# Kernel tuning notes

Measured on AMD Instinct MI355X. Metric: run time of the kernel, lower is better.

## Reference

```python
import jax, jax.numpy as jnp
import numpy as np

N = 100000      # nodes
E = 1600000     # edges (avg degree 16)
DIN = 128       # input_dim
DH = 128        # hidden_dim


def setup_inputs() -> dict:
    key = jax.random.key(0)
    ks = jax.random.split(key, 8)
    x = jax.random.normal(ks[0], (N, DIN), dtype=jnp.float32)
    edge_index = jax.random.randint(ks[1], (2, E), 0, N, dtype=jnp.int32)
    s_in = 1.0 / np.sqrt(DIN)
    s_h = 1.0 / np.sqrt(DH)
    # PyG SAGEConv: out = lin_l(mean_aggr(x_src)) + lin_r(x_dst); lin_l has bias, lin_r does not.
    w1l = jax.random.normal(ks[2], (DIN, DH), dtype=jnp.float32) * s_in
    b1l = jnp.zeros((DH,), dtype=jnp.float32)
    w1r = jax.random.normal(ks[3], (DIN, DH), dtype=jnp.float32) * s_in
    w2l = jax.random.normal(ks[4], (DH, DH), dtype=jnp.float32) * s_h
    b2l = jnp.zeros((DH,), dtype=jnp.float32)
    w2r = jax.random.normal(ks[5], (DH, DH), dtype=jnp.float32) * s_h
    return {"x": x, "edge_index": edge_index, "w1l": w1l, "b1l": b1l,
            "w1r": w1r, "w2l": w2l, "b2l": b2l, "w2r": w2r}


def sage_conv(x, edge_index, wl, bl, wr):
    # edge_index[0] = source, edge_index[1] = target (PyG source_to_target flow)
    row, col = edge_index[0], edge_index[1]
    num_nodes = x.shape[0]
    agg = jax.ops.segment_sum(x[row], col, num_segments=num_nodes)          # [N, d]
    deg = jax.ops.segment_sum(jnp.ones((row.shape[0],), x.dtype), col,
                              num_segments=num_nodes)                        # [N]
    mean = agg / jnp.maximum(deg, 1.0)[:, None]
    return mean @ wl + bl + x @ wr


def reference(x, edge_index, w1l, b1l, w1r, w2l, b2l, w2r):
    h = jax.nn.relu(sage_conv(x, edge_index, w1l, b1l, w1r))
    return jax.nn.relu(sage_conv(h, edge_index, w2l, b2l, w2r))
```

## Files before the change

kernel.cpp:

```cpp
#include <hip/hip_runtime.h>

#define D 128
#define BM 128
#define NWG 256

typedef short short8 __attribute__((ext_vector_type(8)));
typedef float f32x4 __attribute__((ext_vector_type(4)));

__device__ inline unsigned short f2bf_rne(float x) {
    unsigned int b = __float_as_uint(x);
    unsigned int r = (b + 0x7FFFu + ((b >> 16) & 1u)) >> 16;
    return (unsigned short)r;
}
__device__ inline float bf2f(unsigned short h) {
    return __uint_as_float(((unsigned int)h) << 16);
}
__device__ inline void acc_bf(float4& a, ushort4 u) {
    a.x += __uint_as_float((unsigned int)u.x << 16);
    a.y += __uint_as_float((unsigned int)u.y << 16);
    a.z += __uint_as_float((unsigned int)u.z << 16);
    a.w += __uint_as_float((unsigned int)u.w << 16);
}

__global__ __launch_bounds__(256) void convert_x(const float* __restrict__ x,
                                                 unsigned short* __restrict__ xb,
                                                 int total) {
    int i = (blockIdx.x * 256 + threadIdx.x) * 8;
    if (i < total) {
        float4 a = *reinterpret_cast<const float4*>(x + i);
        float4 b = *reinterpret_cast<const float4*>(x + i + 4);
        ushort4 u0, u1;
        u0.x = f2bf_rne(a.x); u0.y = f2bf_rne(a.y); u0.z = f2bf_rne(a.z); u0.w = f2bf_rne(a.w);
        u1.x = f2bf_rne(b.x); u1.y = f2bf_rne(b.y); u1.z = f2bf_rne(b.z); u1.w = f2bf_rne(b.w);
        *reinterpret_cast<ushort4*>(xb + i) = u0;
        *reinterpret_cast<ushort4*>(xb + i + 4) = u1;
    }
}


__global__ void scan1(const int* __restrict__ in, int* __restrict__ out,
                      int* __restrict__ bsum, int n) {
    __shared__ int s[256];
    int t = threadIdx.x;
    int i = blockIdx.x * 256 + t;
    int v = (i < n) ? in[i] : 0;
    s[t] = v;
    __syncthreads();
    #pragma unroll
    for (int off = 1; off < 256; off <<= 1) {
        int add = (t >= off) ? s[t - off] : 0;
        __syncthreads();
        s[t] += add;
        __syncthreads();
    }
    if (i < n) out[i] = s[t] - v;
    if (t == 255) bsum[blockIdx.x] = s[255];
}

__global__ void scan2(int* __restrict__ bsum, int nb) {
    __shared__ int s[512];
    int t = threadIdx.x;
    int v = (t < nb) ? bsum[t] : 0;
    s[t] = v;
    __syncthreads();
    #pragma unroll
    for (int off = 1; off < 512; off <<= 1) {
        int add = (t >= off) ? s[t - off] : 0;
        __syncthreads();
        s[t] += add;
        __syncthreads();
    }
    if (t < nb) bsum[t] = s[t] - v;
}

__global__ void scan3b(int* __restrict__ out, const int* __restrict__ bsum, int n) {
    int i = blockIdx.x * blockDim.x + threadIdx.x;
    if (i < n) out[i] += bsum[i >> 8];
}

__global__ void set_end(int* __restrict__ row_ptr, int n, int e) {
    row_ptr[n] = e;
}


__global__ __launch_bounds__(256) void hist_bucket(const int* __restrict__ coli,
                                                   int* __restrict__ hist_t,
                                                   int e, int nbkt, int cpw) {
    __shared__ int hist[512];
    int w = blockIdx.x, tid = threadIdx.x;
    for (int b = tid; b < nbkt; b += 256) hist[b] = 0;
    __syncthreads();
    int i1 = min((w + 1) * cpw, e);
    for (int i = w * cpw + tid; i < i1; i += 256)
        atomicAdd(&hist[coli[i] >> 8], 1);
    __syncthreads();
    for (int b = tid; b < nbkt; b += 256) hist_t[b * NWG + w] = hist[b];
}

__global__ __launch_bounds__(256) void scatter_bucket(const int* __restrict__ rowi,
                                                      const int* __restrict__ coli,
                                                      const int* __restrict__ scanned,
                                                      unsigned int* __restrict__ ebuf,
                                                      int e, int nbkt, int cpw) {
    __shared__ int cur[512];
    int w = blockIdx.x, tid = threadIdx.x;
    for (int b = tid; b < nbkt; b += 256) cur[b] = scanned[b * NWG + w];
    __syncthreads();
    int i1 = min((w + 1) * cpw, e);
    for (int i = w * cpw + tid; i < i1; i += 256) {
        int c = coli[i];
        int b = c >> 8;
        int p = atomicAdd(&cur[b], 1);
        ebuf[p] = ((unsigned int)rowi[i] << 8) | (unsigned int)(c & 255);
    }
}

__global__ __launch_bounds__(256) void csr_bucket(const int* __restrict__ scanned,
                                                  const unsigned int* __restrict__ ebuf,
                                                  int* __restrict__ row_ptr,
                                                  int* __restrict__ srcs,
                                                  int e, int n, int nbkt) {
    __shared__ int cnt[256], s[256], cur[256];
    int b = blockIdx.x, tid = threadIdx.x;
    int S = scanned[b * NWG];
    int Send = (b == nbkt - 1) ? e : scanned[(b + 1) * NWG];
    cnt[tid] = 0;
    __syncthreads();
    for (int i = S + tid; i < Send; i += 256)
        atomicAdd(&cnt[ebuf[i] & 255], 1);
    __syncthreads();
    int v = cnt[tid];
    s[tid] = v;
    __syncthreads();
    #pragma unroll
    for (int off = 1; off < 256; off <<= 1) {
        int add = (tid >= off) ? s[tid - off] : 0;
        __syncthreads();
        s[tid] += add;
        __syncthreads();
    }
    int offx = s[tid] - v;
    int node = b * 256 + tid;
    if (node < n) row_ptr[node] = S + offx;
    cur[tid] = offx;
    __syncthreads();
    for (int i = S + tid; i < Send; i += 256) {
        unsigned int pe = ebuf[i];
        int lc = (int)(pe & 255u);
        int p = S + atomicAdd(&cur[lc], 1);
        srcs[p] = (int)(pe >> 8);
    }
}

__global__ __launch_bounds__(256) void aggregate_mean_bf16(
    const unsigned short* __restrict__ xb, float* __restrict__ mean,
    const int* __restrict__ row_ptr, const int* __restrict__ srcs, int n) {
    int node = blockIdx.x * 4 + (threadIdx.x >> 6);
    if (node >= n) return;
    int lane = threadIdx.x & 63;
    int half = lane >> 5;
    int l32 = lane & 31;
    int beg = row_ptr[node];
    int end = row_ptr[node + 1];

    float4 ac[8];
    #pragma unroll
    for (int k = 0; k < 8; ++k) ac[k] = make_float4(0.f, 0.f, 0.f, 0.f);

    int j = beg;
    for (; j + 16 <= end; j += 16) {
        int sr[8];
        #pragma unroll
        for (int k = 0; k < 8; ++k) sr[k] = srcs[j + 2 * k + half];
        ushort4 v[8];
        #pragma unroll
        for (int k = 0; k < 8; ++k)
            v[k] = *reinterpret_cast<const ushort4*>(xb + (size_t)sr[k] * D + l32 * 4);
        #pragma unroll
        for (int k = 0; k < 8; ++k) acc_bf(ac[k], v[k]);
    }
    if (j + 8 <= end) {
        int sr[4];
        #pragma unroll
        for (int k = 0; k < 4; ++k) sr[k] = srcs[j + 2 * k + half];
        ushort4 v[4];
        #pragma unroll
        for (int k = 0; k < 4; ++k)
            v[k] = *reinterpret_cast<const ushort4*>(xb + (size_t)sr[k] * D + l32 * 4);
        #pragma unroll
        for (int k = 0; k < 4; ++k) acc_bf(ac[k], v[k]);
        j += 8;
    }
    if (j + 4 <= end) {
        ushort4 v0 = *reinterpret_cast<const ushort4*>(xb + (size_t)srcs[j + half] * D + l32 * 4);
        ushort4 v1 = *reinterpret_cast<const ushort4*>(xb + (size_t)srcs[j + 2 + half] * D + l32 * 4);
        acc_bf(ac[0], v0);
        acc_bf(ac[1], v1);
        j += 4;
    }
    if (j + 2 <= end) {
        ushort4 v0 = *reinterpret_cast<const ushort4*>(xb + (size_t)srcs[j + half] * D + l32 * 4);
        acc_bf(ac[0], v0);
        j += 2;
    }
    if (j < end && half == 0) {
        ushort4 v0 = *reinterpret_cast<const ushort4*>(xb + (size_t)srcs[j] * D + l32 * 4);
        acc_bf(ac[0], v0);
    }
    #pragma unroll
    for (int k = 4; k >= 1; k >>= 1)
        #pragma unroll
        for (int m = 0; m < k; ++m) {
            ac[m].x += ac[m + k].x; ac[m].y += ac[m + k].y;
            ac[m].z += ac[m + k].z; ac[m].w += ac[m + k].w;
        }
    ac[0].x += __shfl_xor(ac[0].x, 32, 64);
    ac[0].y += __shfl_xor(ac[0].y, 32, 64);
    ac[0].z += __shfl_xor(ac[0].z, 32, 64);
    ac[0].w += __shfl_xor(ac[0].w, 32, 64);

    if (half == 0) {
        float inv = 1.0f / fmaxf((float)(end - beg), 1.0f);
        float4 o;
        o.x = ac[0].x * inv; o.y = ac[0].y * inv; o.z = ac[0].z * inv; o.w = ac[0].w * inv;
        *reinterpret_cast<float4*>(mean + (size_t)node * D + l32 * 4) = o;
    }
}

__global__ __launch_bounds__(256) void split_w(const float* __restrict__ w1l,
                                               const float* __restrict__ w1r,
                                               const float* __restrict__ w2l,
                                               const float* __restrict__ w2r,
                                               short* __restrict__ wt) {
    int b = blockIdx.x;
    int layer = b >> 7;
    int nn = b & 127;
    int k = threadIdx.x;
    const float* wl = layer ? w2l : w1l;
    const float* wr = layer ? w2r : w1r;
    float v = (k < 128) ? wl[k * D + nn] : wr[(k - 128) * D + nn];
    unsigned short h = f2bf_rne(v);
    float lo = v - bf2f(h);
    unsigned short l = f2bf_rne(lo);
    short* base = wt + layer * 65536;
    base[nn * 256 + k] = (short)h;
    base[32768 + nn * 256 + k] = (short)l;
}

__global__ __launch_bounds__(256, 2) void sage_mm_mfma(
    const float* __restrict__ mean, const float* __restrict__ xin,
    const short* __restrict__ wth, const short* __restrict__ wtl,
    const float* __restrict__ bias, float* __restrict__ out,
    unsigned short* __restrict__ hbout, int n) {
    __shared__ short sAh[128 * 40];
    __shared__ short sAl[128 * 40];
    __shared__ short sBh[128 * 40];
    __shared__ short sBl[128 * 40];
    const int tid = threadIdx.x;
    const int wave = tid >> 6;
    const int lane = tid & 63;
    const int l15 = lane & 15;
    const int kg = lane >> 4;
    const int row0 = blockIdx.x * BM;

    f32x4 acc[2][8];
    #pragma unroll
    for (int fr = 0; fr < 2; ++fr)
        #pragma unroll
        for (int fc = 0; fc < 8; ++fc)
            acc[fr][fc] = (f32x4){0.f, 0.f, 0.f, 0.f};

    float4 pa[4];
    int4 pbh[2], pbl[2];

    #pragma unroll
    for (int i = 0; i < 4; ++i) {
        int f = tid + i * 256;
        int row = f >> 3, k4 = f & 7;
        int gr = row0 + row;
        pa[i] = (gr < n) ? *reinterpret_cast<const float4*>(&mean[(size_t)gr * D + k4 * 4])
                         : make_float4(0.f, 0.f, 0.f, 0.f);
    }
    #pragma unroll
    for (int i = 0; i < 2; ++i) {
        int f = tid + i * 256;
        int n_ = f >> 2, kq = f & 3;
        pbh[i] = *reinterpret_cast<const int4*>(&wth[n_ * 256 + kq * 8]);
        pbl[i] = *reinterpret_cast<const int4*>(&wtl[n_ * 256 + kq * 8]);
    }

    for (int c = 0; c < 8; ++c) {
        #pragma unroll
        for (int i = 0; i < 4; ++i) {
            int f = tid + i * 256;
            int row = f >> 3, k4 = f & 7;
            const float* pv = &pa[i].x;
            unsigned short h[4], l[4];
            #pragma unroll
            for (int j = 0; j < 4; ++j) {
                float v = pv[j];
                h[j] = f2bf_rne(v);
                l[j] = f2bf_rne(v - bf2f(h[j]));
            }
            short* dsth = &sAh[row * 40 + k4 * 4];
            short* dstl = &sAl[row * 40 + k4 * 4];
            #pragma unroll
            for (int j = 0; j < 4; ++j) { dsth[j] = (short)h[j]; dstl[j] = (short)l[j]; }
        }
        #pragma unroll
        for (int i = 0; i < 2; ++i) {
            int f = tid + i * 256;
            int n_ = f >> 2, kq = f & 3;
            *reinterpret_cast<int4*>(&sBh[n_ * 40 + kq * 8]) = pbh[i];
            *reinterpret_cast<int4*>(&sBl[n_ * 40 + kq * 8]) = pbl[i];
        }
        __syncthreads();

        if (c < 7) {
            const float* __restrict__ anext = (c + 1 < 4) ? mean : xin;
            const int ka = ((c + 1) & 3) * 32;
            const int kb = (c + 1) * 32;
            #pragma unroll
            for (int i = 0; i < 4; ++i) {
                int f = tid + i * 256;
                int row = f >> 3, k4 = f & 7;
                int gr = row0 + row;
                pa[i] = (gr < n) ? *reinterpret_cast<const float4*>(&anext[(size_t)gr * D + ka + k4 * 4])
                                 : make_float4(0.f, 0.f, 0.f, 0.f);
            }
            #pragma unroll
            for (int i = 0; i < 2; ++i) {
                int f = tid + i * 256;
                int n_ = f >> 2, kq = f & 3;
                pbh[i] = *reinterpret_cast<const int4*>(&wth[n_ * 256 + kb + kq * 8]);
                pbl[i] = *reinterpret_cast<const int4*>(&wtl[n_ * 256 + kb + kq * 8]);
            }
        }

        short8 ah[2], al[2];
        #pragma unroll
        for (int fr = 0; fr < 2; ++fr) {
            int r = wave * 32 + fr * 16 + l15;
            ah[fr] = *reinterpret_cast<const short8*>(&sAh[r * 40 + kg * 8]);
            al[fr] = *reinterpret_cast<const short8*>(&sAl[r * 40 + kg * 8]);
        }
        #pragma unroll
        for (int fc = 0; fc < 8; ++fc) {
            int cc = fc * 16 + l15;
            short8 bh = *reinterpret_cast<const short8*>(&sBh[cc * 40 + kg * 8]);
            short8 bl = *reinterpret_cast<const short8*>(&sBl[cc * 40 + kg * 8]);
            #pragma unroll
            for (int fr = 0; fr < 2; ++fr) {
                acc[fr][fc] = __builtin_amdgcn_mfma_f32_16x16x32_bf16(ah[fr], bh, acc[fr][fc], 0, 0, 0);
                acc[fr][fc] = __builtin_amdgcn_mfma_f32_16x16x32_bf16(al[fr], bh, acc[fr][fc], 0, 0, 0);
                acc[fr][fc] = __builtin_amdgcn_mfma_f32_16x16x32_bf16(ah[fr], bl, acc[fr][fc], 0, 0, 0);
            }
        }
        __syncthreads();
    }

    float bz[8];
    #pragma unroll
    for (int fc = 0; fc < 8; ++fc) bz[fc] = bias[fc * 16 + l15];
    #pragma unroll
    for (int fr = 0; fr < 2; ++fr) {
        #pragma unroll
        for (int j = 0; j < 4; ++j) {
            int gr = row0 + wave * 32 + fr * 16 + kg * 4 + j;
            if (gr < n) {
                #pragma unroll
                for (int fc = 0; fc < 8; ++fc) {
                    float v = fmaxf(acc[fr][fc][j] + bz[fc], 0.f);
                    out[(size_t)gr * D + fc * 16 + l15] = v;
                    if (hbout) hbout[(size_t)gr * D + fc * 16 + l15] = f2bf_rne(v);
                }
            }
        }
    }
}


extern "C" void kernel_launch(void* const* d_in, const int* in_sizes, int n_in,
                              void* d_out, int out_size, void* d_ws, size_t ws_size,
                              hipStream_t stream) {
    const float* x   = (const float*)d_in[0];
    const int*   ei  = (const int*)d_in[1];
    const float* w1l = (const float*)d_in[2];
    const float* b1l = (const float*)d_in[3];
    const float* w1r = (const float*)d_in[4];
    const float* w2l = (const float*)d_in[5];
    const float* b2l = (const float*)d_in[6];
    const float* w2r = (const float*)d_in[7];
    float* out = (float*)d_out;

    const int n = in_sizes[0] / D;
    const int e = in_sizes[1] / 2;
    const int* rowi = ei;
    const int* coli = ei + e;

    const int nbkt = (n + 255) >> 8;
    const int n2 = nbkt * NWG;
    const int cpw = (e + NWG - 1) / NWG;
    const int nb2 = n2 / 256;
    const int PN = ((n + 1 + 63) / 64) * 64;
    const int total = n * D;

    int* row_ptr  = (int*)d_ws;
    int* hist_t   = row_ptr + PN;
    int* scanned  = hist_t + n2;
    int* bsum     = scanned + n2;
    int* srcs     = bsum + 512;
    short* wt     = (short*)(srcs + e);
    float* mean   = (float*)(wt + 4 * 32768);
    unsigned short* xhb = (unsigned short*)(mean + (size_t)total);
    unsigned int* ebuf  = (unsigned int*)mean;

    convert_x<<<(total / 8 + 255) / 256, 256, 0, stream>>>(x, xhb, total);
    split_w<<<256, 256, 0, stream>>>(w1l, w1r, w2l, w2r, wt);

    hist_bucket<<<NWG, 256, 0, stream>>>(coli, hist_t, e, nbkt, cpw);
    scan1<<<nb2, 256, 0, stream>>>(hist_t, scanned, bsum, n2);
    scan2<<<1, 512, 0, stream>>>(bsum, nb2);
    scan3b<<<nb2, 256, 0, stream>>>(scanned, bsum, n2);
    scatter_bucket<<<NWG, 256, 0, stream>>>(rowi, coli, scanned, ebuf, e, nbkt, cpw);
    csr_bucket<<<nbkt, 256, 0, stream>>>(scanned, ebuf, row_ptr, srcs, e, n, nbkt);
    set_end<<<1, 1, 0, stream>>>(row_ptr, n, e);

    const int mm_grid = (n + BM - 1) / BM;

    aggregate_mean_bf16<<<(n + 3) / 4, 256, 0, stream>>>(xhb, mean, row_ptr, srcs, n);
    sage_mm_mfma<<<mm_grid, 256, 0, stream>>>(mean, x, wt, wt + 32768, b1l, out, xhb, n);

    aggregate_mean_bf16<<<(n + 3) / 4, 256, 0, stream>>>(xhb, mean, row_ptr, srcs, n);
    sage_mm_mfma<<<mm_grid, 256, 0, stream>>>(mean, out, wt + 65536, wt + 98304, b2l, out, nullptr, n);
}
```

Baseline: 442.1 us.

## Fuse neighbor mean aggregation into the MFMA SAGE GEMM kernel

Merges the gather-mean kernel and the split-bf16 MFMA GEMM into one kernel per layer. Each block aggregates 64 node rows straight into LDS as hi/lo bf16, so the fp32 mean buffer is never written to or read back from global memory. Layer 1 now stores its output only as hi/lo bf16 pairs, which layer 2 consumes directly, and the block tile shrinks to 64 rows with transposed MFMA operands so the epilogue can use vectorized stores. The costs are less GEMM reuse per block and a gather phase and MFMA phase that are serialized inside each block, which may hurt latency hiding.

```diff
diff --git a/kernel.cpp b/kernel.cpp
--- a/kernel.cpp
+++ b/kernel.cpp
@@ -1,7 +1,9 @@
 #include <hip/hip_runtime.h>
 
 #define D 128
-#define BM 128
+#define BM 64
+#define LDM 136
+#define LDC 40
 #define NWG 256
 
 typedef short short8 __attribute__((ext_vector_type(8)));
@@ -149,81 +151,6 @@
         int lc = (int)(pe & 255u);
         int p = S + atomicAdd(&cur[lc], 1);
         srcs[p] = (int)(pe >> 8);
-    }
-}
-
-__global__ __launch_bounds__(256) void aggregate_mean_bf16(
-    const unsigned short* __restrict__ xb, float* __restrict__ mean,
-    const int* __restrict__ row_ptr, const int* __restrict__ srcs, int n) {
-    int node = blockIdx.x * 4 + (threadIdx.x >> 6);
-    if (node >= n) return;
-    int lane = threadIdx.x & 63;
-    int half = lane >> 5;
-    int l32 = lane & 31;
-    int beg = row_ptr[node];
-    int end = row_ptr[node + 1];
-
-    float4 ac[8];
-    #pragma unroll
-    for (int k = 0; k < 8; ++k) ac[k] = make_float4(0.f, 0.f, 0.f, 0.f);
-
-    int j = beg;
-    for (; j + 16 <= end; j += 16) {
-        int sr[8];
-        #pragma unroll
-        for (int k = 0; k < 8; ++k) sr[k] = srcs[j + 2 * k + half];
-        ushort4 v[8];
-        #pragma unroll
-        for (int k = 0; k < 8; ++k)
-            v[k] = *reinterpret_cast<const ushort4*>(xb + (size_t)sr[k] * D + l32 * 4);
-        #pragma unroll
-        for (int k = 0; k < 8; ++k) acc_bf(ac[k], v[k]);
-    }
-    if (j + 8 <= end) {
-        int sr[4];
-        #pragma unroll
-        for (int k = 0; k < 4; ++k) sr[k] = srcs[j + 2 * k + half];
-        ushort4 v[4];
-        #pragma unroll
-        for (int k = 0; k < 4; ++k)
-            v[k] = *reinterpret_cast<const ushort4*>(xb + (size_t)sr[k] * D + l32 * 4);
-        #pragma unroll
-        for (int k = 0; k < 4; ++k) acc_bf(ac[k], v[k]);
-        j += 8;
-    }
-    if (j + 4 <= end) {
-        ushort4 v0 = *reinterpret_cast<const ushort4*>(xb + (size_t)srcs[j + half] * D + l32 * 4);
-        ushort4 v1 = *reinterpret_cast<const ushort4*>(xb + (size_t)srcs[j + 2 + half] * D + l32 * 4);
-        acc_bf(ac[0], v0);
-        acc_bf(ac[1], v1);
-        j += 4;
-    }
-    if (j + 2 <= end) {
-        ushort4 v0 = *reinterpret_cast<const ushort4*>(xb + (size_t)srcs[j + half] * D + l32 * 4);
-        acc_bf(ac[0], v0);
-        j += 2;
-    }
-    if (j < end && half == 0) {
-        ushort4 v0 = *reinterpret_cast<const ushort4*>(xb + (size_t)srcs[j] * D + l32 * 4);
-        acc_bf(ac[0], v0);
-    }
-    #pragma unroll
-    for (int k = 4; k >= 1; k >>= 1)
-        #pragma unroll
-        for (int m = 0; m < k; ++m) {
-            ac[m].x += ac[m + k].x; ac[m].y += ac[m + k].y;
-            ac[m].z += ac[m + k].z; ac[m].w += ac[m + k].w;
-        }
-    ac[0].x += __shfl_xor(ac[0].x, 32, 64);
-    ac[0].y += __shfl_xor(ac[0].y, 32, 64);
-    ac[0].z += __shfl_xor(ac[0].z, 32, 64);
-    ac[0].w += __shfl_xor(ac[0].w, 32, 64);
-
-    if (half == 0) {
-        float inv = 1.0f / fmaxf((float)(end - beg), 1.0f);
-        float4 o;
-        o.x = ac[0].x * inv; o.y = ac[0].y * inv; o.z = ac[0].z * inv; o.w = ac[0].w * inv;
-        *reinterpret_cast<float4*>(mean + (size_t)node * D + l32 * 4) = o;
     }
 }
 
@@ -247,40 +174,30 @@
     base[32768 + nn * 256 + k] = (short)l;
 }
 
-__global__ __launch_bounds__(256, 2) void sage_mm_mfma(
-    const float* __restrict__ mean, const float* __restrict__ xin,
+__global__ __launch_bounds__(256, 2) void fused_sage(
+    const unsigned short* __restrict__ gsrc,
+    const float* __restrict__ xf,
+    const unsigned short* __restrict__ xh,
+    const unsigned short* __restrict__ xl,
     const short* __restrict__ wth, const short* __restrict__ wtl,
-    const float* __restrict__ bias, float* __restrict__ out,
-    unsigned short* __restrict__ hbout, int n) {
-    __shared__ short sAh[128 * 40];
-    __shared__ short sAl[128 * 40];
-    __shared__ short sBh[128 * 40];
-    __shared__ short sBl[128 * 40];
+    const float* __restrict__ bias,
+    const int* __restrict__ row_ptr, const int* __restrict__ srcs,
+    float* __restrict__ outf,
+    unsigned short* __restrict__ hh, unsigned short* __restrict__ hl,
+    int n) {
+    __shared__ unsigned short mh[BM * LDM], ml[BM * LDM];
+    __shared__ short sAh[BM * LDC], sAl[BM * LDC];
+    __shared__ short sBh[128 * LDC], sBl[128 * LDC];
     const int tid = threadIdx.x;
     const int wave = tid >> 6;
     const int lane = tid & 63;
     const int l15 = lane & 15;
     const int kg = lane >> 4;
+    const int half = lane >> 5;
+    const int l32 = lane & 31;
     const int row0 = blockIdx.x * BM;
 
-    f32x4 acc[2][8];
-    #pragma unroll
-    for (int fr = 0; fr < 2; ++fr)
-        #pragma unroll
-        for (int fc = 0; fc < 8; ++fc)
-            acc[fr][fc] = (f32x4){0.f, 0.f, 0.f, 0.f};
-
-    float4 pa[4];
     int4 pbh[2], pbl[2];
-
-    #pragma unroll
-    for (int i = 0; i < 4; ++i) {
-        int f = tid + i * 256;
-        int row = f >> 3, k4 = f & 7;
-        int gr = row0 + row;
-        pa[i] = (gr < n) ? *reinterpret_cast<const float4*>(&mean[(size_t)gr * D + k4 * 4])
-                         : make_float4(0.f, 0.f, 0.f, 0.f);
-    }
     #pragma unroll
     for (int i = 0; i < 2; ++i) {
         int f = tid + i * 256;
@@ -289,45 +206,126 @@
         pbl[i] = *reinterpret_cast<const int4*>(&wtl[n_ * 256 + kq * 8]);
     }
 
+    for (int rr = 0; rr < 16; ++rr) {
+        int r = wave * 16 + rr;
+        int gr = row0 + r;
+        if (gr < n) {
+            int beg = row_ptr[gr];
+            int end = row_ptr[gr + 1];
+            float4 ac[8];
+            #pragma unroll
+            for (int k = 0; k < 8; ++k) ac[k] = make_float4(0.f, 0.f, 0.f, 0.f);
+            int j = beg;
+            for (; j + 16 <= end; j += 16) {
+                int sr[8];
+                #pragma unroll
+                for (int k = 0; k < 8; ++k) sr[k] = srcs[j + 2 * k + half];
+                ushort4 v[8];
+                #pragma unroll
+                for (int k = 0; k < 8; ++k)
+                    v[k] = *reinterpret_cast<const ushort4*>(gsrc + (size_t)sr[k] * D + l32 * 4);
+                #pragma unroll
+                for (int k = 0; k < 8; ++k) acc_bf(ac[k], v[k]);
+            }
+            if (j + 8 <= end) {
+                int sr[4];
+                #pragma unroll
+                for (int k = 0; k < 4; ++k) sr[k] = srcs[j + 2 * k + half];
+                ushort4 v[4];
+                #pragma unroll
+                for (int k = 0; k < 4; ++k)
+                    v[k] = *reinterpret_cast<const ushort4*>(gsrc + (size_t)sr[k] * D + l32 * 4);
+                #pragma unroll
+                for (int k = 0; k < 4; ++k) acc_bf(ac[k], v[k]);
+                j += 8;
+            }
+            if (j + 4 <= end) {
+                ushort4 v0 = *reinterpret_cast<const ushort4*>(gsrc + (size_t)srcs[j + half] * D + l32 * 4);
+                ushort4 v1 = *reinterpret_cast<const ushort4*>(gsrc + (size_t)srcs[j + 2 + half] * D + l32 * 4);
+                acc_bf(ac[0], v0);
+                acc_bf(ac[1], v1);
+                j += 4;
+            }
+            if (j + 2 <= end) {
+                ushort4 v0 = *reinterpret_cast<const ushort4*>(gsrc + (size_t)srcs[j + half] * D + l32 * 4);
+                acc_bf(ac[0], v0);
+                j += 2;
+            }
+            if (j < end && half == 0) {
+                ushort4 v0 = *reinterpret_cast<const ushort4*>(gsrc + (size_t)srcs[j] * D + l32 * 4);
+                acc_bf(ac[0], v0);
+            }
+            #pragma unroll
+            for (int k = 4; k >= 1; k >>= 1)
+                #pragma unroll
+                for (int m = 0; m < k; ++m) {
+                    ac[m].x += ac[m + k].x; ac[m].y += ac[m + k].y;
+                    ac[m].z += ac[m + k].z; ac[m].w += ac[m + k].w;
+                }
+            ac[0].x += __shfl_xor(ac[0].x, 32, 64);
+            ac[0].y += __shfl_xor(ac[0].y, 32, 64);
+            ac[0].z += __shfl_xor(ac[0].z, 32, 64);
+            ac[0].w += __shfl_xor(ac[0].w, 32, 64);
+            if (half == 0) {
+                float inv = 1.0f / fmaxf((float)(end - beg), 1.0f);
+                float m0 = ac[0].x * inv, m1 = ac[0].y * inv;
+                float m2 = ac[0].z * inv, m3 = ac[0].w * inv;
+                ushort4 uh, ul;
+                uh.x = f2bf_rne(m0); ul.x = f2bf_rne(m0 - bf2f(uh.x));
+                uh.y = f2bf_rne(m1); ul.y = f2bf_rne(m1 - bf2f(uh.y));
+                uh.z = f2bf_rne(m2); ul.z = f2bf_rne(m2 - bf2f(uh.z));
+                uh.w = f2bf_rne(m3); ul.w = f2bf_rne(m3 - bf2f(uh.w));
+                *reinterpret_cast<ushort4*>(&mh[r * LDM + l32 * 4]) = uh;
+                *reinterpret_cast<ushort4*>(&ml[r * LDM + l32 * 4]) = ul;
+            }
+        } else if (half == 0) {
+            ushort4 z = {0, 0, 0, 0};
+            *reinterpret_cast<ushort4*>(&mh[r * LDM + l32 * 4]) = z;
+            *reinterpret_cast<ushort4*>(&ml[r * LDM + l32 * 4]) = z;
+        }
+    }
+    __syncthreads();
+
+    f32x4 acc[8];
+    #pragma unroll
+    for (int fc = 0; fc < 8; ++fc) acc[fc] = (f32x4){0.f, 0.f, 0.f, 0.f};
+
+    float4 pda[2];
+    int4 pdh, pdl;
+
     for (int c = 0; c < 8; ++c) {
-        #pragma unroll
-        for (int i = 0; i < 4; ++i) {
-            int f = tid + i * 256;
-            int row = f >> 3, k4 = f & 7;
-            const float* pv = &pa[i].x;
-            unsigned short h[4], l[4];
-            #pragma unroll
-            for (int j = 0; j < 4; ++j) {
-                float v = pv[j];
-                h[j] = f2bf_rne(v);
-                l[j] = f2bf_rne(v - bf2f(h[j]));
-            }
-            short* dsth = &sAh[row * 40 + k4 * 4];
-            short* dstl = &sAl[row * 40 + k4 * 4];
-            #pragma unroll
-            for (int j = 0; j < 4; ++j) { dsth[j] = (short)h[j]; dstl[j] = (short)l[j]; }
-        }
         #pragma unroll
         for (int i = 0; i < 2; ++i) {
             int f = tid + i * 256;
             int n_ = f >> 2, kq = f & 3;
-            *reinterpret_cast<int4*>(&sBh[n_ * 40 + kq * 8]) = pbh[i];
-            *reinterpret_cast<int4*>(&sBl[n_ * 40 + kq * 8]) = pbl[i];
+            *reinterpret_cast<int4*>(&sBh[n_ * LDC + kq * 8]) = pbh[i];
+            *reinterpret_cast<int4*>(&sBl[n_ * LDC + kq * 8]) = pbl[i];
+        }
+        if (c >= 4) {
+            if (xf) {
+                #pragma unroll
+                for (int i = 0; i < 2; ++i) {
+                    int f = tid + i * 256;
+                    int row = f >> 3, k4 = f & 7;
+                    const float* pv = &pda[i].x;
+                    #pragma unroll
+                    for (int j = 0; j < 4; ++j) {
+                        float v = pv[j];
+                        unsigned short h = f2bf_rne(v);
+                        sAh[row * LDC + k4 * 4 + j] = (short)h;
+                        sAl[row * LDC + k4 * 4 + j] = (short)f2bf_rne(v - bf2f(h));
+                    }
+                }
+            } else {
+                int row = tid >> 2, c8 = (tid & 3) * 8;
+                *reinterpret_cast<int4*>(&sAh[row * LDC + c8]) = pdh;
+                *reinterpret_cast<int4*>(&sAl[row * LDC + c8]) = pdl;
+            }
         }
         __syncthreads();
 
         if (c < 7) {
-            const float* __restrict__ anext = (c + 1 < 4) ? mean : xin;
-            const int ka = ((c + 1) & 3) * 32;
             const int kb = (c + 1) * 32;
-            #pragma unroll
-            for (int i = 0; i < 4; ++i) {
-                int f = tid + i * 256;
-                int row = f >> 3, k4 = f & 7;
-                int gr = row0 + row;
-                pa[i] = (gr < n) ? *reinterpret_cast<const float4*>(&anext[(size_t)gr * D + ka + k4 * 4])
-                                 : make_float4(0.f, 0.f, 0.f, 0.f);
-            }
             #pragma unroll
             for (int i = 0; i < 2; ++i) {
                 int f = tid + i * 256;
@@ -335,45 +333,77 @@
                 pbh[i] = *reinterpret_cast<const int4*>(&wth[n_ * 256 + kb + kq * 8]);
                 pbl[i] = *reinterpret_cast<const int4*>(&wtl[n_ * 256 + kb + kq * 8]);
             }
-        }
-
-        short8 ah[2], al[2];
-        #pragma unroll
-        for (int fr = 0; fr < 2; ++fr) {
-            int r = wave * 32 + fr * 16 + l15;
-            ah[fr] = *reinterpret_cast<const short8*>(&sAh[r * 40 + kg * 8]);
-            al[fr] = *reinterpret_cast<const short8*>(&sAl[r * 40 + kg * 8]);
+            if (c + 1 >= 4) {
+                const int k0 = (c + 1 - 4) * 32;
+                if (xf) {
+                    #pragma unroll
+                    for (int i = 0; i < 2; ++i) {
+                        int f = tid + i * 256;
+                        int row = f >> 3, k4 = f & 7;
+                        int gr = row0 + row;
+                        pda[i] = (gr < n) ? *reinterpret_cast<const float4*>(&xf[(size_t)gr * D + k0 + k4 * 4])
+                                          : make_float4(0.f, 0.f, 0.f, 0.f);
+                    }
+                } else {
+                    int row = tid >> 2, c8 = (tid & 3) * 8;
+                    int gr = row0 + row;
+                    if (gr < n) {
+                        pdh = *reinterpret_cast<const int4*>(&xh[(size_t)gr * D + k0 + c8]);
+                        pdl = *reinterpret_cast<const int4*>(&xl[(size_t)gr * D + k0 + c8]);
+                    } else {
+                        pdh = make_int4(0, 0, 0, 0);
+                        pdl = make_int4(0, 0, 0, 0);
+                    }
+                }
+            }
+        }
+
+        short8 ah, al;
+        {
+            int r = wave * 16 + l15;
+            if (c < 4) {
+                ah = *reinterpret_cast<const short8*>(&mh[r * LDM + c * 32 + kg * 8]);
+                al = *reinterpret_cast<const short8*>(&ml[r * LDM + c * 32 + kg * 8]);
+            } else {
+                ah = *reinterpret_cast<const short8*>(&sAh[r * LDC + kg * 8]);
+                al = *reinterpret_cast<const short8*>(&sAl[r * LDC + kg * 8]);
+            }
         }
         #pragma unroll
         for (int fc = 0; fc < 8; ++fc) {
             int cc = fc * 16 + l15;
-            short8 bh = *reinterpret_cast<const short8*>(&sBh[cc * 40 + kg * 8]);
-            short8 bl = *reinterpret_cast<const short8*>(&sBl[cc * 40 + kg * 8]);
-            #pragma unroll
-            for (int fr = 0; fr < 2; ++fr) {
-                acc[fr][fc] = __builtin_amdgcn_mfma_f32_16x16x32_bf16(ah[fr], bh, acc[fr][fc], 0, 0, 0);
-                acc[fr][fc] = __builtin_amdgcn_mfma_f32_16x16x32_bf16(al[fr], bh, acc[fr][fc], 0, 0, 0);
-                acc[fr][fc] = __builtin_amdgcn_mfma_f32_16x16x32_bf16(ah[fr], bl, acc[fr][fc], 0, 0, 0);
-            }
-        }
-        __syncthreads();
-    }
-
-    float bz[8];
-    #pragma unroll
-    for (int fc = 0; fc < 8; ++fc) bz[fc] = bias[fc * 16 + l15];
-    #pragma unroll
-    for (int fr = 0; fr < 2; ++fr) {
+            short8 bh = *reinterpret_cast<const short8*>(&sBh[cc * LDC + kg * 8]);
+            short8 bl = *reinterpret_cast<const short8*>(&sBl[cc * LDC + kg * 8]);
+            acc[fc] = __builtin_amdgcn_mfma_f32_16x16x32_bf16(bh, ah, acc[fc], 0, 0, 0);
+            acc[fc] = __builtin_amdgcn_mfma_f32_16x16x32_bf16(bh, al, acc[fc], 0, 0, 0);
+            acc[fc] = __builtin_amdgcn_mfma_f32_16x16x32_bf16(bl, ah, acc[fc], 0, 0, 0);
+        }
+        __syncthreads();
+    }
+
+    float4 b4[8];
+    #pragma unroll
+    for (int fc = 0; fc < 8; ++fc)
+        b4[fc] = *reinterpret_cast<const float4*>(&bias[fc * 16 + kg * 4]);
+    int gr = row0 + wave * 16 + l15;
+    if (gr < n) {
         #pragma unroll
-        for (int j = 0; j < 4; ++j) {
-            int gr = row0 + wave * 32 + fr * 16 + kg * 4 + j;
-            if (gr < n) {
-                #pragma unroll
-                for (int fc = 0; fc < 8; ++fc) {
-                    float v = fmaxf(acc[fr][fc][j] + bz[fc], 0.f);
-                    out[(size_t)gr * D + fc * 16 + l15] = v;
-                    if (hbout) hbout[(size_t)gr * D + fc * 16 + l15] = f2bf_rne(v);
-                }
+        for (int fc = 0; fc < 8; ++fc) {
+            float4 o;
+            o.x = fmaxf(acc[fc][0] + b4[fc].x, 0.f);
+            o.y = fmaxf(acc[fc][1] + b4[fc].y, 0.f);
+            o.z = fmaxf(acc[fc][2] + b4[fc].z, 0.f);
+            o.w = fmaxf(acc[fc][3] + b4[fc].w, 0.f);
+            size_t base = (size_t)gr * D + fc * 16 + kg * 4;
+            if (outf) *reinterpret_cast<float4*>(&outf[base]) = o;
+            if (hh) {
+                ushort4 uh, ul;
+                uh.x = f2bf_rne(o.x); ul.x = f2bf_rne(o.x - bf2f(uh.x));
+                uh.y = f2bf_rne(o.y); ul.y = f2bf_rne(o.y - bf2f(uh.y));
+                uh.z = f2bf_rne(o.z); ul.z = f2bf_rne(o.z - bf2f(uh.z));
+                uh.w = f2bf_rne(o.w); ul.w = f2bf_rne(o.w - bf2f(uh.w));
+                *reinterpret_cast<ushort4*>(&hh[base]) = uh;
+                *reinterpret_cast<ushort4*>(&hl[base]) = ul;
             }
         }
     }
@@ -411,9 +441,10 @@
     int* bsum     = scanned + n2;
     int* srcs     = bsum + 512;
     short* wt     = (short*)(srcs + e);
-    float* mean   = (float*)(wt + 4 * 32768);
-    unsigned short* xhb = (unsigned short*)(mean + (size_t)total);
-    unsigned int* ebuf  = (unsigned int*)mean;
+    unsigned short* xhb = (unsigned short*)(wt + 4 * 32768);
+    unsigned short* hhb = xhb + (size_t)total;
+    unsigned short* hlb = hhb + (size_t)total;
+    unsigned int* ebuf  = (unsigned int*)hhb;
 
     convert_x<<<(total / 8 + 255) / 256, 256, 0, stream>>>(x, xhb, total);
     split_w<<<256, 256, 0, stream>>>(w1l, w1r, w2l, w2r, wt);
@@ -426,11 +457,13 @@
     csr_bucket<<<nbkt, 256, 0, stream>>>(scanned, ebuf, row_ptr, srcs, e, n, nbkt);
     set_end<<<1, 1, 0, stream>>>(row_ptr, n, e);
 
-    const int mm_grid = (n + BM - 1) / BM;
-
-    aggregate_mean_bf16<<<(n + 3) / 4, 256, 0, stream>>>(xhb, mean, row_ptr, srcs, n);
-    sage_mm_mfma<<<mm_grid, 256, 0, stream>>>(mean, x, wt, wt + 32768, b1l, out, xhb, n);
-
-    aggregate_mean_bf16<<<(n + 3) / 4, 256, 0, stream>>>(xhb, mean, row_ptr, srcs, n);
-    sage_mm_mfma<<<mm_grid, 256, 0, stream>>>(mean, out, wt + 65536, wt + 98304, b2l, out, nullptr, n);
-}
+    const int grid = (n + BM - 1) / BM;
+
+    fused_sage<<<grid, 256, 0, stream>>>(xhb, x, nullptr, nullptr,
+                                         wt, wt + 32768, b1l, row_ptr, srcs,
+                                         nullptr, hhb, hlb, n);
+
+    fused_sage<<<grid, 256, 0, stream>>>(hhb, nullptr, hhb, hlb,
+                                         wt + 65536, wt + 98304, b2l, row_ptr, srcs,
+                                         out, nullptr, nullptr, n);
+}
```

New measurement: 591.5 us. 1.34x slower.
